# Kernel tuning notes

Hardware: AMD Instinct MI355X
Metric: run time of the kernel (lower is better)

The kernel has to match this reference:

```python
import jax, jax.numpy as jnp
import numpy as np

B, N, C = 32, 8732, 81  # batch, SSD300 anchors, COCO classes incl. background


def setup_inputs() -> dict:
    key = jax.random.key(0)
    k1, k2, k3, k4, k5 = jax.random.split(key, 5)
    ploc = jax.random.normal(k1, (B, N, 4), jnp.float32)
    plabel = jax.random.normal(k2, (B, N, C), jnp.float32)
    gloc = jax.random.normal(k3, (B, N, 4), jnp.float32)
    labels = jax.random.randint(k4, (B, N), 1, C)
    is_pos = jax.random.uniform(k5, (B, N)) < 0.02
    glabel = jnp.where(is_pos, labels, 0).astype(jnp.int32)
    return {"ploc": ploc, "plabel": plabel, "gloc": gloc, "glabel": glabel}


def _smooth_l1(x):
    ax = jnp.abs(x)
    return jnp.where(ax < 1.0, 0.5 * ax * ax, ax - 0.5)


def reference(ploc, plabel, gloc, glabel):
    num_classes = plabel.shape[-1]
    mask = glabel.reshape(-1) > 0                      # [B*N] positive anchors
    pos_num = mask.sum()

    # Localization loss: SmoothL1 summed over 4 coords, only on positives
    loss_l = _smooth_l1(ploc.reshape(-1, 4) - gloc.reshape(-1, 4)).sum(axis=1)
    loss_l = (mask.astype(loss_l.dtype) * loss_l).sum()

    # Per-anchor cross entropy over flattened batch
    logp = jax.nn.log_softmax(plabel.reshape(-1, num_classes), axis=-1)
    gt = glabel.reshape(-1)
    loss_c = -jnp.take_along_axis(logp, gt[:, None], axis=1)[:, 0]  # [B*N]

    # Hard negative mining via double argsort (rank of each anchor's CE loss)
    con_neg = jnp.where(mask, 0.0, loss_c)
    con_idx = jnp.argsort(-con_neg)        # descending sort indices
    con_rank = jnp.argsort(con_idx)        # rank of each element
    neg_num = jnp.minimum(3 * pos_num, mask.shape[0])
    neg_mask = con_rank < neg_num

    closs = (loss_c * (mask.astype(loss_c.dtype) + neg_mask.astype(loss_c.dtype))).sum()
    total_loss = loss_l + closs
    return jnp.where(pos_num > 0, total_loss / pos_num.astype(total_loss.dtype), 0.0)
```

## Files before the change

kernel.cpp:

```cpp
#include <hip/hip_runtime.h>
#include <math.h>

#define M_TOTAL (32 * 8732)
#define M4      (M_TOTAL / 4)
#define NBLK_A  (M_TOTAL / 64)
#define NBLK_S  273
#define NREP    8

#define CON_B    ((size_t)0)
#define HISTR_B  ((size_t)M_TOTAL * 4)
#define H1_B     (HISTR_B + (size_t)NREP * 2048 * 4)
#define H2_B     (H1_B + (size_t)2048 * 4)
#define G_B      (H2_B + (size_t)1024 * 4)
#define PART_B   (G_B + 128)
#define ZERO_WORDS ((NREP * 2048 * 4 + 2048 * 4 + 1024 * 4 + 128) / 4)

struct GS {
    unsigned pn;
    float    lossl;
    float    poslc;
    unsigned b0;
    unsigned k1;
    unsigned pref;
    unsigned k2;
    float    sumhi0;
    float    sumhi1;
};

__device__ __forceinline__ float smooth_l1(float d) {
    float ad = fabsf(d);
    return (ad < 1.0f) ? 0.5f * ad * ad : ad - 0.5f;
}

#define GLLDS16(gp, lp) __builtin_amdgcn_global_load_lds( \
    (__attribute__((address_space(1))) void*)(gp),        \
    (__attribute__((address_space(3))) void*)(lp), 16, 0, 0)

__device__ void selectk256(const unsigned* cnt, int nbins, unsigned k,
                           unsigned* ssum, unsigned* pbin, unsigned* pk) {
    const int t = threadIdx.x;
    const int chunk = nbins >> 8;
    if (t == 0) { *pbin = 0u; *pk = 0u; }
    unsigned tot = 0;
    for (int j = 0; j < chunk; ++j) tot += cnt[t * chunk + j];
    ssum[t] = tot;
    __syncthreads();
    for (int off = 1; off < 256; off <<= 1) {
        const unsigned val = ssum[t];
        const unsigned add = (t + off < 256) ? ssum[t + off] : 0u;
        __syncthreads();
        ssum[t] = val + add;
        __syncthreads();
    }
    const unsigned s_after = (t < 255) ? ssum[t + 1] : 0u;
    if (k > 0u && ssum[t] >= k && k > s_after) {
        unsigned cum = s_after;
        for (int j = chunk - 1; j >= 0; --j) {
            const unsigned bin = t * chunk + j;
            const unsigned nc = cum + cnt[bin];
            if (nc >= k) { *pbin = bin; *pk = k - cum; break; }
            cum = nc;
        }
    }
    __syncthreads();
}

__global__ __launch_bounds__(256) void kA(const float* __restrict__ ploc,
                                          const float* __restrict__ plabel,
                                          const float* __restrict__ gloc,
                                          const int* __restrict__ glabel,
                                          float* __restrict__ con,
                                          unsigned* __restrict__ zbase,
                                          float4* __restrict__ part) {
    __shared__ __align__(16) float stage[4 * 1296];
    __shared__ float rf[4][3];

    const int tid  = threadIdx.x;
    const int w    = tid >> 6;
    const int lane = tid & 63;
    const int g    = lane >> 2;
    const int l    = lane & 3;

    if (blockIdx.x < 77) {
        const int zi = blockIdx.x * 256 + tid;
        if (zi < ZERO_WORDS) zbase[zi] = 0u;
    }

    const size_t wrow0 = (size_t)blockIdx.x * 64 + (size_t)w * 16;
    const char*  gsrc  = (const char*)(plabel + wrow0 * 81);
    char*        ldst  = (char*)&stage[w * 1296];
#pragma unroll
    for (int j = 0; j < 5; ++j)
        GLLDS16(gsrc + (size_t)j * 1024 + (size_t)lane * 16, ldst + j * 1024);
    if (lane < 4)
        GLLDS16(gsrc + 5120 + (size_t)lane * 16, ldst + 5120);

    const size_t row = wrow0 + g;
    const float pl = ploc[wrow0 * 4 + lane];
    const float gl = gloc[wrow0 * 4 + lane];
    int gt = 0;
    if (l == 0) gt = glabel[row];
    const int mask = gt > 0;

    float s = smooth_l1(pl - gl);
    s += __shfl_xor(s, 1);
    s += __shfl_xor(s, 2);

    __syncthreads();

    const float* rowp = &stage[w * 1296 + g * 81];
    float v[20];
    float m = -INFINITY;
#pragma unroll
    for (int j = 0; j < 20; ++j) { v[j] = rowp[j * 4 + l]; m = fmaxf(m, v[j]); }
    float v80 = 0.0f;
    if (l == 0) { v80 = rowp[80]; m = fmaxf(m, v80); }
    m = fmaxf(m, __shfl_xor(m, 1));
    m = fmaxf(m, __shfl_xor(m, 2));

    float e = 0.0f;
#pragma unroll
    for (int j = 0; j < 20; ++j) e += __expf(v[j] - m);
    if (l == 0) e += __expf(v80 - m);
    e += __shfl_xor(e, 1);
    e += __shfl_xor(e, 2);
    const float lse = m + __logf(e);

    float wl = 0.f, wc = 0.f, wp = 0.f;
    if (l == 0) {
        const float x_gt   = rowp[gt];
        const float loss_c = lse - x_gt;
        const float cn     = mask ? 0.0f : fmaxf(loss_c, 0.0f);
        con[row] = cn;
        if (mask) { wl = s; wc = loss_c; wp = 1.0f; }
    }
#pragma unroll
    for (int off = 4; off < 64; off <<= 1) {
        wl += __shfl_xor(wl, off);
        wc += __shfl_xor(wc, off);
        wp += __shfl_xor(wp, off);
    }
    if (lane == 0) { rf[w][0] = wl; rf[w][1] = wc; rf[w][2] = wp; }
    __syncthreads();

    if (tid == 0)
        part[blockIdx.x] = make_float4(rf[0][0] + rf[1][0] + rf[2][0] + rf[3][0],
                                       rf[0][1] + rf[1][1] + rf[2][1] + rf[3][1],
                                       rf[0][2] + rf[1][2] + rf[2][2] + rf[3][2], 0.f);
}

__global__ __launch_bounds__(256) void kB(const float4* __restrict__ con4,
                                          unsigned* __restrict__ histR,
                                          const float4* __restrict__ part,
                                          GS* __restrict__ G) {
    __shared__ unsigned lh[2048];
    __shared__ float    rf3[4][3];
    const int tid = threadIdx.x;

    for (int i = tid; i < 2048; i += 256) lh[i] = 0u;
    __syncthreads();

    const int i = blockIdx.x * 256 + tid;
    if (i < M4) {
        const float4 q = con4[i];
        atomicAdd(&lh[__float_as_uint(q.x) >> 21], 1u);
        atomicAdd(&lh[__float_as_uint(q.y) >> 21], 1u);
        atomicAdd(&lh[__float_as_uint(q.z) >> 21], 1u);
        atomicAdd(&lh[__float_as_uint(q.w) >> 21], 1u);
    }
    __syncthreads();

    unsigned* hrep = histR + (size_t)(blockIdx.x & (NREP - 1)) * 2048;
    for (int b = tid; b < 2048; b += 256) {
        const unsigned c = lh[b];
        if (c) atomicAdd(&hrep[b], c);
    }

    if (blockIdx.x == 0) {
        float sl = 0.f, sc = 0.f, sp = 0.f;
        for (int p = tid; p < NBLK_A; p += 256) {
            const float4 q = part[p];
            sl += q.x; sc += q.y; sp += q.z;
        }
#pragma unroll
        for (int off = 1; off < 64; off <<= 1) {
            sl += __shfl_xor(sl, off); sc += __shfl_xor(sc, off); sp += __shfl_xor(sp, off);
        }
        if ((tid & 63) == 0) { rf3[tid >> 6][0] = sl; rf3[tid >> 6][1] = sc; rf3[tid >> 6][2] = sp; }
        __syncthreads();
        if (tid == 0) {
            const float tsl = rf3[0][0] + rf3[1][0] + rf3[2][0] + rf3[3][0];
            const float tsc = rf3[0][1] + rf3[1][1] + rf3[2][1] + rf3[3][1];
            const float tsp = rf3[0][2] + rf3[1][2] + rf3[2][2] + rf3[3][2];
            G->pn = (unsigned)(tsp + 0.5f);
            G->lossl = tsl;
            G->poslc = tsc;
        }
    }
}

__global__ __launch_bounds__(256) void kC(const float4* __restrict__ con4,
                                          const unsigned* __restrict__ histR,
                                          unsigned* __restrict__ h1,
                                          GS* __restrict__ G) {
    __shared__ unsigned lh[2048];
    __shared__ unsigned ssum[256];
    __shared__ unsigned sbin, sk;
    __shared__ float    wred[4];
    const int tid = threadIdx.x;

    for (int b = tid; b < 2048; b += 256) {
        unsigned c = 0;
#pragma unroll
        for (int r = 0; r < NREP; ++r) c += histR[r * 2048 + b];
        lh[b] = c;
    }
    __syncthreads();

    const unsigned pn = G->pn;
    unsigned k0 = 3u * pn;
    if (k0 > (unsigned)M_TOTAL) k0 = (unsigned)M_TOTAL;
    selectk256(lh, 2048, k0, ssum, &sbin, &sk);
    const unsigned b0 = sbin, k1loc = sk;

    const int i = blockIdx.x * 256 + tid;
    float s = 0.f;
    if (i < M4) {
        const float4 q = con4[i];
        const float xs[4] = {q.x, q.y, q.z, q.w};
#pragma unroll
        for (int j = 0; j < 4; ++j) {
            const unsigned u  = __float_as_uint(xs[j]);
            const unsigned hi = u >> 21;
            if (hi > b0) s += xs[j];
            else if (hi == b0) atomicAdd(&h1[(u >> 10) & 0x7FFu], 1u);
        }
    }
#pragma unroll
    for (int off = 1; off < 64; off <<= 1) s += __shfl_xor(s, off);
    if ((tid & 63) == 0) wred[tid >> 6] = s;
    __syncthreads();
    if (tid == 0) {
        const float tot = wred[0] + wred[1] + wred[2] + wred[3];
        if (tot != 0.f) atomicAdd(&G->sumhi0, tot);
        if (blockIdx.x == 0) { G->b0 = b0; G->k1 = k1loc; }
    }
}

__global__ __launch_bounds__(256) void kD(const float4* __restrict__ con4,
                                          const unsigned* __restrict__ h1,
                                          unsigned* __restrict__ h2,
                                          GS* __restrict__ G) {
    __shared__ unsigned lh[2048];
    __shared__ unsigned ssum[256];
    __shared__ unsigned sbin, sk;
    __shared__ float    wred[4];
    const int tid = threadIdx.x;

    for (int b = tid; b < 2048; b += 256) lh[b] = h1[b];
    __syncthreads();

    const unsigned b0 = G->b0;
    const unsigned k1 = G->k1;
    selectk256(lh, 2048, k1, ssum, &sbin, &sk);
    const unsigned b1 = sbin, k2loc = sk;

    const int i = blockIdx.x * 256 + tid;
    float s = 0.f;
    if (i < M4) {
        const float4 q = con4[i];
        const float xs[4] = {q.x, q.y, q.z, q.w};
#pragma unroll
        for (int j = 0; j < 4; ++j) {
            const unsigned u = __float_as_uint(xs[j]);
            if ((u >> 21) == b0) {
                const unsigned mid = (u >> 10) & 0x7FFu;
                if (mid > b1) s += xs[j];
                else if (mid == b1) atomicAdd(&h2[u & 0x3FFu], 1u);
            }
        }
    }
#pragma unroll
    for (int off = 1; off < 64; off <<= 1) s += __shfl_xor(s, off);
    if ((tid & 63) == 0) wred[tid >> 6] = s;
    __syncthreads();
    if (tid == 0) {
        const float tot = wred[0] + wred[1] + wred[2] + wred[3];
        if (tot != 0.f) atomicAdd(&G->sumhi1, tot);
        if (blockIdx.x == 0) { G->pref = (b0 << 11) | b1; G->k2 = k2loc; }
    }
}

__global__ __launch_bounds__(256) void kE(const unsigned* __restrict__ h2,
                                          const GS* __restrict__ G,
                                          float* __restrict__ out) {
    __shared__ unsigned lh[1024];
    __shared__ unsigned ssum[256];
    __shared__ unsigned sbin, sk;
    __shared__ float    wred[4];
    const int tid = threadIdx.x;

    for (int b = tid; b < 1024; b += 256) lh[b] = h2[b];
    __syncthreads();
    const unsigned pref = G->pref;
    const unsigned k2   = G->k2;
    selectk256(lh, 1024, k2, ssum, &sbin, &sk);
    const unsigned ct = sbin, r = sk;

    float s2 = 0.f;
    for (int b = tid; b < 1024; b += 256) {
        const unsigned c = lh[b];
        if ((unsigned)b > ct && c)
            s2 += (float)c * __uint_as_float((pref << 10) | (unsigned)b);
    }
#pragma unroll
    for (int off = 1; off < 64; off <<= 1) s2 += __shfl_xor(s2, off);
    if ((tid & 63) == 0) wred[tid >> 6] = s2;
    __syncthreads();

    if (tid == 0) {
        const float sumhi2 = wred[0] + wred[1] + wred[2] + wred[3];
        const unsigned pn = G->pn;
        float outv = 0.f;
        if (pn > 0u) {
            const float tval  = __uint_as_float((pref << 10) | ct);
            const float closs = G->poslc + G->sumhi0 + G->sumhi1 + sumhi2 + (float)r * tval;
            outv = (G->lossl + closs) / (float)pn;
        }
        out[0] = outv;
    }
}

extern "C" void kernel_launch(void* const* d_in, const int* in_sizes, int n_in,
                              void* d_out, int out_size, void* d_ws, size_t ws_size,
                              hipStream_t stream) {
    const float* ploc   = (const float*)d_in[0];
    const float* plabel = (const float*)d_in[1];
    const float* gloc   = (const float*)d_in[2];
    const int*   glabel = (const int*)d_in[3];
    float* out = (float*)d_out;
    char*  ws  = (char*)d_ws;

    float*    con   = (float*)(ws + CON_B);
    unsigned* histR = (unsigned*)(ws + HISTR_B);
    unsigned* h1    = (unsigned*)(ws + H1_B);
    unsigned* h2    = (unsigned*)(ws + H2_B);
    GS*       G     = (GS*)(ws + G_B);
    float4*   part  = (float4*)(ws + PART_B);

    kA<<<NBLK_A, 256, 0, stream>>>(ploc, plabel, gloc, glabel, con,
                                   (unsigned*)(ws + HISTR_B), part);
    kB<<<NBLK_S, 256, 0, stream>>>((const float4*)con, histR, part, G);
    kC<<<NBLK_S, 256, 0, stream>>>((const float4*)con, histR, h1, G);
    kD<<<NBLK_S, 256, 0, stream>>>((const float4*)con, h1, h2, G);
    kE<<<1, 256, 0, stream>>>(h2, G, out);
}
```

Before: 178.9 us.

## Fuse coarse histogram into CE kernel and drop separate histogram pass

Each kA block now builds a shared-memory coarse histogram of the negative CE losses as it writes them and flushes it into replicated global histograms, so the separate kB pass is removed. Replication goes from 8 to 16 copies to spread contention from the larger number of flushing blocks. The partial-sum reduction moves into every kC block, and workspace zeroing moves to a hipMemsetAsync before kA. This saves one launch and one full re-read of the con array, at the cost of extra global atomics from 4366 blocks and a memset node.

```diff
diff --git a/kernel.cpp b/kernel.cpp
--- a/kernel.cpp
+++ b/kernel.cpp
@@ -5,7 +5,7 @@
 #define M4      (M_TOTAL / 4)
 #define NBLK_A  (M_TOTAL / 64)
 #define NBLK_S  273
-#define NREP    8
+#define NREP    16
 
 #define CON_B    ((size_t)0)
 #define HISTR_B  ((size_t)M_TOTAL * 4)
@@ -13,7 +13,7 @@
 #define H2_B     (H1_B + (size_t)2048 * 4)
 #define G_B      (H2_B + (size_t)1024 * 4)
 #define PART_B   (G_B + 128)
-#define ZERO_WORDS ((NREP * 2048 * 4 + 2048 * 4 + 1024 * 4 + 128) / 4)
+#define ZERO_BYTES ((size_t)NREP * 2048 * 4 + 2048 * 4 + 1024 * 4 + 128)
 
 struct GS {
     unsigned pn;
@@ -70,9 +70,10 @@
                                           const float* __restrict__ gloc,
                                           const int* __restrict__ glabel,
                                           float* __restrict__ con,
-                                          unsigned* __restrict__ zbase,
+                                          unsigned* __restrict__ histR,
                                           float4* __restrict__ part) {
     __shared__ __align__(16) float stage[4 * 1296];
+    __shared__ unsigned lh[2048];
     __shared__ float rf[4][3];
 
     const int tid  = threadIdx.x;
@@ -81,10 +82,7 @@
     const int g    = lane >> 2;
     const int l    = lane & 3;
 
-    if (blockIdx.x < 77) {
-        const int zi = blockIdx.x * 256 + tid;
-        if (zi < ZERO_WORDS) zbase[zi] = 0u;
-    }
+    for (int i = tid; i < 2048; i += 256) lh[i] = 0u;
 
     const size_t wrow0 = (size_t)blockIdx.x * 64 + (size_t)w * 16;
     const char*  gsrc  = (const char*)(plabel + wrow0 * 81);
@@ -132,6 +130,7 @@
         const float loss_c = lse - x_gt;
         const float cn     = mask ? 0.0f : fmaxf(loss_c, 0.0f);
         con[row] = cn;
+        atomicAdd(&lh[__float_as_uint(cn) >> 21], 1u);
         if (mask) { wl = s; wc = loss_c; wp = 1.0f; }
     }
 #pragma unroll
@@ -147,66 +146,24 @@
         part[blockIdx.x] = make_float4(rf[0][0] + rf[1][0] + rf[2][0] + rf[3][0],
                                        rf[0][1] + rf[1][1] + rf[2][1] + rf[3][1],
                                        rf[0][2] + rf[1][2] + rf[2][2] + rf[3][2], 0.f);
-}
-
-__global__ __launch_bounds__(256) void kB(const float4* __restrict__ con4,
-                                          unsigned* __restrict__ histR,
-                                          const float4* __restrict__ part,
-                                          GS* __restrict__ G) {
-    __shared__ unsigned lh[2048];
-    __shared__ float    rf3[4][3];
-    const int tid = threadIdx.x;
-
-    for (int i = tid; i < 2048; i += 256) lh[i] = 0u;
-    __syncthreads();
-
-    const int i = blockIdx.x * 256 + tid;
-    if (i < M4) {
-        const float4 q = con4[i];
-        atomicAdd(&lh[__float_as_uint(q.x) >> 21], 1u);
-        atomicAdd(&lh[__float_as_uint(q.y) >> 21], 1u);
-        atomicAdd(&lh[__float_as_uint(q.z) >> 21], 1u);
-        atomicAdd(&lh[__float_as_uint(q.w) >> 21], 1u);
-    }
-    __syncthreads();
 
     unsigned* hrep = histR + (size_t)(blockIdx.x & (NREP - 1)) * 2048;
-    for (int b = tid; b < 2048; b += 256) {
-        const unsigned c = lh[b];
-        if (c) atomicAdd(&hrep[b], c);
-    }
-
-    if (blockIdx.x == 0) {
-        float sl = 0.f, sc = 0.f, sp = 0.f;
-        for (int p = tid; p < NBLK_A; p += 256) {
-            const float4 q = part[p];
-            sl += q.x; sc += q.y; sp += q.z;
-        }
-#pragma unroll
-        for (int off = 1; off < 64; off <<= 1) {
-            sl += __shfl_xor(sl, off); sc += __shfl_xor(sc, off); sp += __shfl_xor(sp, off);
-        }
-        if ((tid & 63) == 0) { rf3[tid >> 6][0] = sl; rf3[tid >> 6][1] = sc; rf3[tid >> 6][2] = sp; }
-        __syncthreads();
-        if (tid == 0) {
-            const float tsl = rf3[0][0] + rf3[1][0] + rf3[2][0] + rf3[3][0];
-            const float tsc = rf3[0][1] + rf3[1][1] + rf3[2][1] + rf3[3][1];
-            const float tsp = rf3[0][2] + rf3[1][2] + rf3[2][2] + rf3[3][2];
-            G->pn = (unsigned)(tsp + 0.5f);
-            G->lossl = tsl;
-            G->poslc = tsc;
-        }
+    for (int i = tid; i < 2048; i += 256) {
+        const unsigned c = lh[i];
+        if (c) atomicAdd(&hrep[i], c);
     }
 }
 
 __global__ __launch_bounds__(256) void kC(const float4* __restrict__ con4,
                                           const unsigned* __restrict__ histR,
+                                          const float4* __restrict__ part,
                                           unsigned* __restrict__ h1,
                                           GS* __restrict__ G) {
     __shared__ unsigned lh[2048];
     __shared__ unsigned ssum[256];
     __shared__ unsigned sbin, sk;
     __shared__ float    wred[4];
+    __shared__ float    rf3[4][3];
     const int tid = threadIdx.x;
 
     for (int b = tid; b < 2048; b += 256) {
@@ -215,11 +172,22 @@
         for (int r = 0; r < NREP; ++r) c += histR[r * 2048 + b];
         lh[b] = c;
     }
-    __syncthreads();
-
-    const unsigned pn = G->pn;
+    float sl = 0.f, sc = 0.f, sp = 0.f;
+    for (int p = tid; p < NBLK_A; p += 256) {
+        const float4 q = part[p];
+        sl += q.x; sc += q.y; sp += q.z;
+    }
+#pragma unroll
+    for (int off = 1; off < 64; off <<= 1) {
+        sl += __shfl_xor(sl, off); sc += __shfl_xor(sc, off); sp += __shfl_xor(sp, off);
+    }
+    if ((tid & 63) == 0) { rf3[tid >> 6][0] = sl; rf3[tid >> 6][1] = sc; rf3[tid >> 6][2] = sp; }
+    __syncthreads();
+    const float tsp = rf3[0][2] + rf3[1][2] + rf3[2][2] + rf3[3][2];
+    const unsigned pn = (unsigned)(tsp + 0.5f);
     unsigned k0 = 3u * pn;
     if (k0 > (unsigned)M_TOTAL) k0 = (unsigned)M_TOTAL;
+
     selectk256(lh, 2048, k0, ssum, &sbin, &sk);
     const unsigned b0 = sbin, k1loc = sk;
 
@@ -243,7 +211,12 @@
     if (tid == 0) {
         const float tot = wred[0] + wred[1] + wred[2] + wred[3];
         if (tot != 0.f) atomicAdd(&G->sumhi0, tot);
-        if (blockIdx.x == 0) { G->b0 = b0; G->k1 = k1loc; }
+        if (blockIdx.x == 0) {
+            G->pn = pn;
+            G->lossl = rf3[0][0] + rf3[1][0] + rf3[2][0] + rf3[3][0];
+            G->poslc = rf3[0][1] + rf3[1][1] + rf3[2][1] + rf3[3][1];
+            G->b0 = b0; G->k1 = k1loc;
+        }
     }
 }
 
@@ -348,10 +321,9 @@
     GS*       G     = (GS*)(ws + G_B);
     float4*   part  = (float4*)(ws + PART_B);
 
-    kA<<<NBLK_A, 256, 0, stream>>>(ploc, plabel, gloc, glabel, con,
-                                   (unsigned*)(ws + HISTR_B), part);
-    kB<<<NBLK_S, 256, 0, stream>>>((const float4*)con, histR, part, G);
-    kC<<<NBLK_S, 256, 0, stream>>>((const float4*)con, histR, h1, G);
+    hipMemsetAsync(ws + HISTR_B, 0, ZERO_BYTES, stream);
+    kA<<<NBLK_A, 256, 0, stream>>>(ploc, plabel, gloc, glabel, con, histR, part);
+    kC<<<NBLK_S, 256, 0, stream>>>((const float4*)con, histR, part, h1, G);
     kD<<<NBLK_S, 256, 0, stream>>>((const float4*)con, h1, h2, G);
     kE<<<1, 256, 0, stream>>>(h2, G, out);
 }
```

After: 174.3 us. 1.03x faster.
